# Kernel optimization log

Hardware: AMD Instinct MI355X
Metric: run time of the kernel (lower is better)

The kernel has to match this reference:

```python
import jax, jax.numpy as jnp
import numpy as np

B, IN, H = 8192, 1024, 1024

def setup_inputs() -> dict:
    key = jax.random.key(0)
    ks = jax.random.split(key, 11)
    s = 1.0 / np.sqrt(IN + H)  # torch Linear default init range
    def W(k):
        return jax.random.uniform(k, (H, IN + H), jnp.float32, -s, s)
    def b(k):
        return jax.random.uniform(k, (H,), jnp.float32, -s, s)
    return {
        "inputs": jax.random.normal(ks[0], (B, IN), jnp.float32),
        "hidden": jax.random.normal(ks[1], (B, H), jnp.float32),
        "c": jax.random.normal(ks[2], (B, H), jnp.float32),
        "Wf": W(ks[3]), "bf": b(ks[4]),
        "Wi": W(ks[5]), "bi": b(ks[6]),
        "Wo": W(ks[7]), "bo": b(ks[8]),
        "Wc": W(ks[9]), "bc": b(ks[10]),
    }

def reference(inputs, hidden, c, Wf, bf, Wi, bi, Wo, bo, Wc, bc):
    # concat order matches torch: [hidden, inputs]
    x = jnp.concatenate([hidden, inputs], axis=1)  # [B, H+IN]
    # fuse the four gate linears into one GEMM: [B, H+IN] x [H+IN, 4H]
    Wall = jnp.concatenate([Wf, Wi, Wo, Wc], axis=0)  # [4H, H+IN]
    ball = jnp.concatenate([bf, bi, bo, bc], axis=0)  # [4H]
    gates = x @ Wall.T + ball                         # [B, 4H]
    f, i, o, c_hat = jnp.split(gates, 4, axis=1)
    f = jax.nn.sigmoid(f)
    i = jax.nn.sigmoid(i)
    o = jax.nn.sigmoid(o)
    c_hat = jnp.tanh(c_hat)
    c_new = f * c + i * c_hat
    h_new = o * jnp.tanh(c_new)
    return (h_new, c_new)
```

## Files before the change

### kernel.cpp

```cpp
#include <hip/hip_runtime.h>
#include <cstdint>

#define Bdim 8192
#define Hdim 1024
#define Kdim 2048
#define BM 128
#define BU 32
#define BK 32

#define XELEMS ((size_t)Bdim * Kdim)
#define WELEMS ((size_t)4 * Hdim * Kdim)
#define WGATE  ((size_t)Hdim * Kdim)

typedef __bf16 bf16;
typedef bf16  bf16x8  __attribute__((ext_vector_type(8)));
typedef float floatx4 __attribute__((ext_vector_type(4)));

typedef __attribute__((address_space(1))) uint32_t gu32;
typedef __attribute__((address_space(3))) uint32_t lu32;

__device__ __forceinline__ void gl_lds16(const bf16* g, bf16* l) {
    __builtin_amdgcn_global_load_lds((gu32*)(bf16*)g, (lu32*)l, 16, 0, 0);
}

__device__ __forceinline__ float sigf(float x) {
    return 1.0f / (1.0f + __expf(-x));
}
__device__ __forceinline__ float tanhfast(float x) {
    return 2.0f / (1.0f + __expf(-2.0f * x)) - 1.0f;
}

__global__ __launch_bounds__(256) void cvt_kernel(
    const float* __restrict__ inp, const float* __restrict__ hid,
    const float* __restrict__ Wf,  const float* __restrict__ Wi,
    const float* __restrict__ Wo,  const float* __restrict__ Wc,
    bf16* __restrict__ xc, bf16* __restrict__ wc)
{
    const size_t id = (size_t)blockIdx.x * 256 + threadIdx.x;
    const size_t e  = id * 8;
    const float* src;
    bf16* dst;
    if (e < XELEMS) {
        const size_t b = e >> 11;
        const size_t k = e & (Kdim - 1);
        src = (k < Hdim) ? (hid + b * Hdim + k) : (inp + b * Hdim + (k - Hdim));
        dst = xc + e;
    } else {
        const size_t w = e - XELEMS;
        const size_t g = w >> 21;
        const float* Ws = (g == 0) ? Wf : (g == 1) ? Wi : (g == 2) ? Wo : Wc;
        src = Ws + (w & (WGATE - 1));
        dst = wc + w;
    }
    const float4 a  = *reinterpret_cast<const float4*>(src);
    const float4 b4 = *reinterpret_cast<const float4*>(src + 4);
    bf16x8 o;
    o[0] = (bf16)a.x;  o[1] = (bf16)a.y;  o[2] = (bf16)a.z;  o[3] = (bf16)a.w;
    o[4] = (bf16)b4.x; o[5] = (bf16)b4.y; o[6] = (bf16)b4.z; o[7] = (bf16)b4.w;
    *reinterpret_cast<bf16x8*>(dst) = o;
}

__global__ __launch_bounds__(256) void lstm_fused(
    const bf16* __restrict__ xc,   const bf16* __restrict__ wc,
    const float* __restrict__ cin,
    const float* __restrict__ bfv, const float* __restrict__ biv,
    const float* __restrict__ bov, const float* __restrict__ bcv,
    float* __restrict__ out)
{
    __shared__ __align__(16) bf16 As[BM * BK];
    __shared__ __align__(16) bf16 Bs[128 * BK];

    const int tid  = threadIdx.x;
    const int lane = tid & 63;
    const int wv   = tid >> 6;
    const int quad = lane >> 4;
    const int l16  = lane & 15;

    const int m0 = blockIdx.x * BM;
    const int u0 = blockIdx.y * BU;

    const int r0   = tid >> 2;
    const int koff = (tid & 3) * 8;

    const bf16* xA0 = xc + (size_t)(m0 + r0) * Kdim + koff;
    const bf16* xA1 = xA0 + (size_t)64 * Kdim;

    const int ul = r0 & 31;
    const int ghalf = (tid & 128) ? 1 : 0;
    const bf16* WB0 = wc + (size_t)(ghalf)     * WGATE + (size_t)(u0 + ul) * Kdim + koff;
    const bf16* WB1 = wc + (size_t)(ghalf + 2) * WGATE + (size_t)(u0 + ul) * Kdim + koff;

    bf16* lA0 = &As[tid * 8];
    bf16* lA1 = &As[(256 + tid) * 8];
    bf16* lB0 = &Bs[tid * 8];
    bf16* lB1 = &Bs[(256 + tid) * 8];

    floatx4 acc[2][2][4] = {};

    for (int k0 = 0; k0 < Kdim; k0 += BK) {
        gl_lds16(xA0 + k0, lA0);
        gl_lds16(xA1 + k0, lA1);
        gl_lds16(WB0 + k0, lB0);
        gl_lds16(WB1 + k0, lB1);
        __syncthreads();

        bf16x8 af[2];
        af[0] = *reinterpret_cast<const bf16x8*>(&As[(wv * 32 +      l16) * BK + quad * 8]);
        af[1] = *reinterpret_cast<const bf16x8*>(&As[(wv * 32 + 16 + l16) * BK + quad * 8]);
        bf16x8 bfr[2][4];
        #pragma unroll
        for (int h = 0; h < 2; ++h)
            #pragma unroll
            for (int g = 0; g < 4; ++g)
                bfr[h][g] = *reinterpret_cast<const bf16x8*>(
                    &Bs[(g * 32 + h * 16 + l16) * BK + quad * 8]);

        #pragma unroll
        for (int a = 0; a < 2; ++a)
            #pragma unroll
            for (int h = 0; h < 2; ++h)
                #pragma unroll
                for (int g = 0; g < 4; ++g)
                    acc[a][h][g] = __builtin_amdgcn_mfma_f32_16x16x32_bf16(
                        af[a], bfr[h][g], acc[a][h][g], 0, 0, 0);
        __syncthreads();
    }

    const int row_base = m0 + wv * 32 + quad * 4;
    #pragma unroll
    for (int h = 0; h < 2; ++h) {
        const int unit = u0 + h * 16 + l16;
        const float bff = bfv[unit];
        const float bii = biv[unit];
        const float boo = bov[unit];
        const float bcc = bcv[unit];
        #pragma unroll
        for (int a = 0; a < 2; ++a) {
            #pragma unroll
            for (int r = 0; r < 4; ++r) {
                const int row = row_base + a * 16 + r;
                const size_t off = (size_t)row * Hdim + unit;
                const float fg = sigf(acc[a][h][0][r] + bff);
                const float ig = sigf(acc[a][h][1][r] + bii);
                const float og = sigf(acc[a][h][2][r] + boo);
                const float ch = tanhfast(acc[a][h][3][r] + bcc);
                const float cn = fg * cin[off] + ig * ch;
                const float hn = og * tanhfast(cn);
                out[off] = hn;
                out[(size_t)Bdim * Hdim + off] = cn;
            }
        }
    }
}

extern "C" void kernel_launch(void* const* d_in, const int* in_sizes, int n_in,
                              void* d_out, int out_size, void* d_ws, size_t ws_size,
                              hipStream_t stream) {
    const float* inputs = (const float*)d_in[0];
    const float* hidden = (const float*)d_in[1];
    const float* cprev  = (const float*)d_in[2];
    const float* Wf     = (const float*)d_in[3];
    const float* bfp    = (const float*)d_in[4];
    const float* Wi     = (const float*)d_in[5];
    const float* bip    = (const float*)d_in[6];
    const float* Wo     = (const float*)d_in[7];
    const float* bop    = (const float*)d_in[8];
    const float* Wc     = (const float*)d_in[9];
    const float* bcp    = (const float*)d_in[10];
    float* out = (float*)d_out;

    const size_t need = (XELEMS + WELEMS) * sizeof(bf16);
    if (ws_size < need) return;
    bf16* xc = (bf16*)d_ws;
    bf16* wc = xc + XELEMS;

    const int cvt_blocks = (int)((XELEMS + WELEMS) / 8 / 256);
    cvt_kernel<<<dim3(cvt_blocks), dim3(256), 0, stream>>>(
        inputs, hidden, Wf, Wi, Wo, Wc, xc, wc);

    dim3 grid(Bdim / BM, Hdim / BU);
    lstm_fused<<<grid, dim3(256), 0, stream>>>(
        xc, wc, cprev, bfp, bip, bop, bcp, out);
}
```

Before: 379.6 us.

## Widen unit tile to 64 with 2x2 wave layout and XOR-swizzled LDS

Doubles the per-block gate-unit tile from 32 to 64, arranging the four waves as a 2x2 grid so each wave computes 64 rows by 32 units across all four gates. This raises arithmetic intensity per LDS tile and halves the number of blocks re-reading the activation matrix. It also adds an XOR swizzle on the 16-byte k-chunks in LDS to reduce bank conflicts on fragment reads. The cost is double the accumulator registers (128 floats per thread) under a 2-blocks-per-SM launch bound, and the loop is still single-buffered.

```diff
diff --git a/kernel.cpp b/kernel.cpp
--- a/kernel.cpp
+++ b/kernel.cpp
@@ -5,7 +5,7 @@
 #define Hdim 1024
 #define Kdim 2048
 #define BM 128
-#define BU 32
+#define BU 64
 #define BK 32
 
 #define XELEMS ((size_t)Bdim * Kdim)
@@ -60,7 +60,7 @@
     *reinterpret_cast<bf16x8*>(dst) = o;
 }
 
-__global__ __launch_bounds__(256) void lstm_fused(
+__global__ __launch_bounds__(256, 2) void lstm_fused(
     const bf16* __restrict__ xc,   const bf16* __restrict__ wc,
     const float* __restrict__ cin,
     const float* __restrict__ bfv, const float* __restrict__ biv,
@@ -68,7 +68,7 @@
     float* __restrict__ out)
 {
     __shared__ __align__(16) bf16 As[BM * BK];
-    __shared__ __align__(16) bf16 Bs[128 * BK];
+    __shared__ __align__(16) bf16 Bs[4 * BU * BK];
 
     const int tid  = threadIdx.x;
     const int lane = tid & 63;
@@ -79,44 +79,61 @@
     const int m0 = blockIdx.x * BM;
     const int u0 = blockIdx.y * BU;
 
-    const int r0   = tid >> 2;
-    const int koff = (tid & 3) * 8;
-
-    const bf16* xA0 = xc + (size_t)(m0 + r0) * Kdim + koff;
-    const bf16* xA1 = xA0 + (size_t)64 * Kdim;
-
-    const int ul = r0 & 31;
-    const int ghalf = (tid & 128) ? 1 : 0;
-    const bf16* WB0 = wc + (size_t)(ghalf)     * WGATE + (size_t)(u0 + ul) * Kdim + koff;
-    const bf16* WB1 = wc + (size_t)(ghalf + 2) * WGATE + (size_t)(u0 + ul) * Kdim + koff;
-
-    bf16* lA0 = &As[tid * 8];
-    bf16* lA1 = &As[(256 + tid) * 8];
-    bf16* lB0 = &Bs[tid * 8];
-    bf16* lB1 = &Bs[(256 + tid) * 8];
-
-    floatx4 acc[2][2][4] = {};
+    const bf16* gA[2];
+    bf16* lA[2];
+    #pragma unroll
+    for (int c = 0; c < 2; ++c) {
+        const int li   = c * 256 + tid;
+        const int row  = li >> 2;
+        const int slot = li & 3;
+        const int gch  = slot ^ ((row >> 1) & 3);
+        gA[c] = xc + (size_t)(m0 + row) * Kdim + gch * 8;
+        lA[c] = &As[li * 8];
+    }
+    const bf16* gB[4];
+    bf16* lB[4];
+    #pragma unroll
+    for (int c = 0; c < 4; ++c) {
+        const int li   = c * 256 + tid;
+        const int nr   = li >> 2;
+        const int slot = li & 3;
+        const int gch  = slot ^ ((nr >> 1) & 3);
+        const int g    = nr >> 6;
+        const int ul   = nr & 63;
+        gB[c] = wc + (size_t)g * WGATE + (size_t)(u0 + ul) * Kdim + gch * 8;
+        lB[c] = &Bs[li * 8];
+    }
+
+    const int kslot = quad ^ ((l16 >> 1) & 3);
+    const int rbase = (wv & 1) * 64;
+    const int ubase = (wv >> 1) * 32;
+
+    floatx4 acc[4][2][4] = {};
 
     for (int k0 = 0; k0 < Kdim; k0 += BK) {
-        gl_lds16(xA0 + k0, lA0);
-        gl_lds16(xA1 + k0, lA1);
-        gl_lds16(WB0 + k0, lB0);
-        gl_lds16(WB1 + k0, lB1);
+        gl_lds16(gA[0] + k0, lA[0]);
+        gl_lds16(gA[1] + k0, lA[1]);
+        gl_lds16(gB[0] + k0, lB[0]);
+        gl_lds16(gB[1] + k0, lB[1]);
+        gl_lds16(gB[2] + k0, lB[2]);
+        gl_lds16(gB[3] + k0, lB[3]);
         __syncthreads();
 
-        bf16x8 af[2];
-        af[0] = *reinterpret_cast<const bf16x8*>(&As[(wv * 32 +      l16) * BK + quad * 8]);
-        af[1] = *reinterpret_cast<const bf16x8*>(&As[(wv * 32 + 16 + l16) * BK + quad * 8]);
+        bf16x8 af[4];
+        #pragma unroll
+        for (int a = 0; a < 4; ++a)
+            af[a] = *reinterpret_cast<const bf16x8*>(
+                &As[(rbase + a * 16 + l16) * BK + kslot * 8]);
         bf16x8 bfr[2][4];
         #pragma unroll
         for (int h = 0; h < 2; ++h)
             #pragma unroll
             for (int g = 0; g < 4; ++g)
                 bfr[h][g] = *reinterpret_cast<const bf16x8*>(
-                    &Bs[(g * 32 + h * 16 + l16) * BK + quad * 8]);
-
-        #pragma unroll
-        for (int a = 0; a < 2; ++a)
+                    &Bs[(g * 64 + ubase + h * 16 + l16) * BK + kslot * 8]);
+
+        #pragma unroll
+        for (int a = 0; a < 4; ++a)
             #pragma unroll
             for (int h = 0; h < 2; ++h)
                 #pragma unroll
@@ -126,19 +143,20 @@
         __syncthreads();
     }
 
-    const int row_base = m0 + wv * 32 + quad * 4;
+    const int m_base = m0 + rbase + quad * 4;
+    const int u_base = u0 + ubase;
     #pragma unroll
     for (int h = 0; h < 2; ++h) {
-        const int unit = u0 + h * 16 + l16;
+        const int unit = u_base + h * 16 + l16;
         const float bff = bfv[unit];
         const float bii = biv[unit];
         const float boo = bov[unit];
         const float bcc = bcv[unit];
         #pragma unroll
-        for (int a = 0; a < 2; ++a) {
+        for (int a = 0; a < 4; ++a) {
             #pragma unroll
             for (int r = 0; r < 4; ++r) {
-                const int row = row_base + a * 16 + r;
+                const int row = m_base + a * 16 + r;
                 const size_t off = (size_t)row * Hdim + unit;
                 const float fg = sigf(acc[a][h][0][r] + bff);
                 const float ig = sigf(acc[a][h][1][r] + bii);
```

Result: faster. 341.5 us (-10.0%).
